# Kernel tuning notes

Measured on AMD Instinct MI355X. Metric: run time of the kernel, lower is better.

## Reference

```python
import jax, jax.numpy as jnp
import numpy as np

B, S, D = 2, 2048, 2048
NH, NKV, HD = 16, 4, 128
EPS = 1e-6


def rmsnorm(x, w, eps=EPS):
    # torch.nn.RMSNorm: x * rsqrt(mean(x^2) + eps) * weight
    ms = jnp.mean(jnp.square(x), axis=-1, keepdims=True)
    return x * jax.lax.rsqrt(ms + eps) * w


def apply_rotary_emb(x, freqs_cis):
    # x: (B, S, H, HD); freqs_cis: (S, HD//2, 2) -> pairwise complex rotation (gpt-fast style)
    xs = x.reshape(*x.shape[:-1], -1, 2)          # (B,S,H,HD//2,2)
    fc = freqs_cis[None, :, None, :, :]           # (1,S,1,HD//2,2)
    xr, xi = xs[..., 0], xs[..., 1]
    fr, fi = fc[..., 0], fc[..., 1]
    out = jnp.stack([xr * fr - xi * fi, xi * fr + xr * fi], axis=-1)
    return out.reshape(x.shape)


def setup_inputs() -> dict:
    key = jax.random.key(0)
    ks = jax.random.split(key, 4)
    x = jax.random.normal(ks[0], (B, S, D), dtype=jnp.float32)
    freqs_cis = jax.random.normal(ks[1], (S, HD // 2, 2), dtype=jnp.float32)
    wqkv = jax.random.normal(ks[2], ((NH + 2 * NKV) * HD, D), dtype=jnp.float32) * (D ** -0.5)
    wo = jax.random.normal(ks[3], (NH * HD, D), dtype=jnp.float32).T * ((NH * HD) ** -0.5)
    wo = jnp.asarray(wo)  # (D, NH*HD) torch layout (out,in)
    q_norm_w = jnp.ones((HD,), dtype=jnp.float32)
    k_norm_w = jnp.ones((HD,), dtype=jnp.float32)
    return {"x": x, "freqs_cis": freqs_cis, "wqkv": wqkv, "wo": wo,
            "q_norm_w": q_norm_w, "k_norm_w": k_norm_w}


def reference(x, freqs_cis, wqkv, wo, q_norm_w, k_norm_w):
    b, s, _ = x.shape
    q_size, kv_size = NH * HD, NKV * HD
    qkv = jnp.einsum('bsd,ed->bse', x, wqkv)  # fused QKV projection
    q, k, v = jnp.split(qkv, [q_size, q_size + kv_size], axis=-1)
    q = q.reshape(b, s, NH, HD)
    k = k.reshape(b, s, NKV, HD)
    v = v.reshape(b, s, NKV, HD)
    q = rmsnorm(q, q_norm_w)
    k = rmsnorm(k, k_norm_w)
    q = apply_rotary_emb(q, freqs_cis)
    k = apply_rotary_emb(k, freqs_cis)
    # GQA: repeat_interleave KV heads to NH
    rep = NH // NKV
    k = jnp.repeat(k, rep, axis=2)  # (b,s,NH,HD)
    v = jnp.repeat(v, rep, axis=2)
    scale = 1.0 / np.sqrt(HD)
    scores = jnp.einsum('bqhd,bkhd->bhqk', q, k) * scale
    causal = jnp.tril(jnp.ones((s, s), dtype=bool))
    scores = jnp.where(causal[None, None], scores, -jnp.inf)
    attn = jax.nn.softmax(scores, axis=-1)
    y = jnp.einsum('bhqk,bkhd->bqhd', attn, v)
    y = y.reshape(b, s, q_size)
    return jnp.einsum('bse,de->bsd', y, wo)
```

## Files before the change

### kernel.cpp

```cpp
#include <hip/hip_runtime.h>
#include <math.h>

constexpr int B_ = 2, S_ = 2048, D_ = 2048, NH_ = 16, NKV_ = 4, HD_ = 128;
constexpr int EQKV_ = (NH_ + 2 * NKV_) * HD_;
constexpr int M_ = B_ * S_;
constexpr float EPS_ = 1e-6f;
constexpr float QSCALE_ = 0.08838834764831845f;

typedef __attribute__((ext_vector_type(8))) short bf16x8;
typedef __attribute__((ext_vector_type(4))) float f32x4;
typedef __attribute__((address_space(1))) unsigned int gu32;
typedef __attribute__((address_space(3))) unsigned int lu32;

__device__ inline ushort f2bf(float f) {
    unsigned u = __float_as_uint(f);
    return (ushort)((u + 0x7FFF + ((u >> 16) & 1)) >> 16);
}

constexpr int NP_X = M_ * D_ / 4;
constexpr int NP_W = EQKV_ * D_ / 4;
constexpr int NP_O = D_ * NH_ * HD_ / 4;
__global__ __launch_bounds__(256) void pack_all(
    const float* __restrict__ x, const float* __restrict__ wqkv,
    const float* __restrict__ wo,
    ushort* __restrict__ xbf, ushort* __restrict__ wqkvbf,
    ushort* __restrict__ wobf)
{
    int i = blockIdx.x * 256 + threadIdx.x;
    const float4* src; ushort4* dst; int j;
    if (i < NP_X)                 { src = (const float4*)x;    dst = (ushort4*)xbf;    j = i; }
    else if (i < NP_X + NP_W)     { src = (const float4*)wqkv; dst = (ushort4*)wqkvbf; j = i - NP_X; }
    else if (i < NP_X + NP_W + NP_O) { src = (const float4*)wo; dst = (ushort4*)wobf;  j = i - NP_X - NP_W; }
    else return;
    float4 f = src[j];
    ushort4 u;
    u.x = f2bf(f.x); u.y = f2bf(f.y); u.z = f2bf(f.z); u.w = f2bf(f.w);
    dst[j] = u;
}

__global__ __launch_bounds__(256) void gemm_nt_bf16(
    const ushort* __restrict__ A, const ushort* __restrict__ W,
    float* __restrict__ C, int M, int N, int K)
{
    __shared__ ushort As[128 * 32];
    __shared__ ushort Bs[128 * 32];
    const int t = threadIdx.x;
    const int wave = t >> 6, lane = t & 63;
    const int nwg = gridDim.x * gridDim.y;
    int wg = blockIdx.y * gridDim.x + blockIdx.x;
    wg = (wg & 7) * (nwg >> 3) + (wg >> 3);
    const int m0 = (wg / gridDim.x) * 128, n0 = (wg % gridDim.x) * 128;
    const int wm = (wave >> 1) * 64, wn = (wave & 1) * 64;
    const int lrow = lane & 15, lquad = lane >> 4;

    f32x4 acc[4][4];
#pragma unroll
    for (int i = 0; i < 4; ++i)
#pragma unroll
        for (int j = 0; j < 4; ++j) acc[i][j] = (f32x4){0.f, 0.f, 0.f, 0.f};

    for (int k0 = 0; k0 < K; k0 += 32) {
        __syncthreads();
#pragma unroll
        for (int i = 0; i < 2; ++i) {
            int chunk = t + 256 * i;
            int row = chunk >> 2, seg = chunk & 3;
            int ubase = (wave * 64 + 256 * i) * 8;
            __builtin_amdgcn_global_load_lds(
                (const gu32*)(A + (size_t)(m0 + row) * K + k0 + seg * 8),
                (lu32*)(As + ubase), 16, 0, 0);
            __builtin_amdgcn_global_load_lds(
                (const gu32*)(W + (size_t)(n0 + row) * K + k0 + seg * 8),
                (lu32*)(Bs + ubase), 16, 0, 0);
        }
        __syncthreads();

        bf16x8 af[4], bf[4];
#pragma unroll
        for (int i = 0; i < 4; ++i) {
            af[i] = *(const bf16x8*)(As + (wm + i * 16 + lrow) * 32 + lquad * 8);
            bf[i] = *(const bf16x8*)(Bs + (wn + i * 16 + lrow) * 32 + lquad * 8);
        }
#pragma unroll
        for (int i = 0; i < 4; ++i)
#pragma unroll
            for (int j = 0; j < 4; ++j)
                acc[i][j] = __builtin_amdgcn_mfma_f32_16x16x32_bf16(
                    af[i], bf[j], acc[i][j], 0, 0, 0);
    }
#pragma unroll
    for (int i = 0; i < 4; ++i)
#pragma unroll
        for (int j = 0; j < 4; ++j) {
            float* cp = C + (size_t)(m0 + wm + i * 16 + lquad * 4) * N
                          + n0 + wn + j * 16 + lrow;
#pragma unroll
            for (int r = 0; r < 4; ++r) cp[(size_t)r * N] = acc[i][j][r];
        }
}

__global__ __launch_bounds__(256) void gemm_qkv_fused(
    const ushort* __restrict__ A,
    const ushort* __restrict__ W,
    const float* __restrict__ freqs,
    const float* __restrict__ qw, const float* __restrict__ kw,
    ushort* __restrict__ qo, ushort* __restrict__ ko, ushort* __restrict__ vo,
    int K)
{
    __shared__ __align__(16) ushort smem[128 * 136];
    __shared__ float rsbuf[256];
    ushort* As = smem;
    ushort* Bs = smem + 4096;
    ushort* Lt = smem;

    const int t = threadIdx.x;
    const int wave = t >> 6, lane = t & 63;
    const int nwg = gridDim.x * gridDim.y;
    int wg = blockIdx.y * gridDim.x + blockIdx.x;
    wg = (wg & 7) * (nwg >> 3) + (wg >> 3);
    const int m0 = (wg / gridDim.x) * 128, n0 = (wg % gridDim.x) * 128;
    const int wm = (wave >> 1) * 64, wn = (wave & 1) * 64;
    const int half = wave & 1;
    const int lrow = lane & 15, lquad = lane >> 4;
    const int head = n0 >> 7;
    const int b = m0 >> 11, s0 = m0 & (S_ - 1);

    f32x4 acc[4][4];
#pragma unroll
    for (int i = 0; i < 4; ++i)
#pragma unroll
        for (int j = 0; j < 4; ++j) acc[i][j] = (f32x4){0.f, 0.f, 0.f, 0.f};

    for (int k0 = 0; k0 < K; k0 += 32) {
        __syncthreads();
#pragma unroll
        for (int i = 0; i < 2; ++i) {
            int chunk = t + 256 * i;
            int row = chunk >> 2, seg = chunk & 3;
            int ubase = (wave * 64 + 256 * i) * 8;
            __builtin_amdgcn_global_load_lds(
                (const gu32*)(A + (size_t)(m0 + row) * K + k0 + seg * 8),
                (lu32*)(As + ubase), 16, 0, 0);
            __builtin_amdgcn_global_load_lds(
                (const gu32*)(W + (size_t)(n0 + row) * K + k0 + seg * 8),
                (lu32*)(Bs + ubase), 16, 0, 0);
        }
        __syncthreads();

        bf16x8 af[4], bf[4];
#pragma unroll
        for (int i = 0; i < 4; ++i) {
            af[i] = *(const bf16x8*)(As + (wm + i * 16 + lrow) * 32 + lquad * 8);
            bf[i] = *(const bf16x8*)(Bs + (wn + i * 16 + lrow) * 32 + lquad * 8);
        }
#pragma unroll
        for (int i = 0; i < 4; ++i)
#pragma unroll
            for (int j = 0; j < 4; ++j)
                acc[i][j] = __builtin_amdgcn_mfma_f32_16x16x32_bf16(
                    af[i], bf[j], acc[i][j], 0, 0, 0);
    }
    __syncthreads();

    float part[4][4];
    if (head < NH_ + NKV_) {
#pragma unroll
        for (int i = 0; i < 4; ++i)
#pragma unroll
            for (int r = 0; r < 4; ++r) {
                float p = acc[i][0][r] * acc[i][0][r]
                        + acc[i][1][r] * acc[i][1][r]
                        + acc[i][2][r] * acc[i][2][r]
                        + acc[i][3][r] * acc[i][3][r];
#pragma unroll
                for (int off = 1; off < 16; off <<= 1) p += __shfl_xor(p, off);
                part[i][r] = p;
                if (lrow == 0)
                    rsbuf[half * 128 + wm + i * 16 + lquad * 4 + r] = p;
            }
    }
    __syncthreads();

    if (head < NH_ + NKV_) {
        const float* nw = (head < NH_) ? qw : kw;
        float wv[4];
#pragma unroll
        for (int j = 0; j < 4; ++j) wv[j] = nw[wn + j * 16 + lrow];
#pragma unroll
        for (int i = 0; i < 4; ++i)
#pragma unroll
            for (int r = 0; r < 4; ++r) {
                const int rowid = wm + i * 16 + lquad * 4 + r;
                const int s = s0 + rowid;
                const float total = part[i][r] + rsbuf[(half ^ 1) * 128 + rowid];
                const float rs = rsqrtf(total * (1.0f / HD_) + EPS_);
#pragma unroll
                for (int j = 0; j < 4; ++j) {
                    const int d = wn + j * 16 + lrow;
                    const float xn = acc[i][j][r] * rs * wv[j];
                    const float other = __shfl_xor(xn, 1);
                    const float fr = freqs[s * HD_ + (d & ~1)];
                    const float fi = freqs[s * HD_ + (d & ~1) + 1];
                    float out = (d & 1) ? fmaf(xn, fr, other * fi)
                                        : fmaf(xn, fr, -other * fi);
                    if (head < NH_) out *= QSCALE_;
                    Lt[rowid * 136 + d] = f2bf(out);
                }
            }
    } else {
#pragma unroll
        for (int i = 0; i < 4; ++i)
#pragma unroll
            for (int j = 0; j < 4; ++j)
#pragma unroll
                for (int r = 0; r < 4; ++r)
                    Lt[(wn + j * 16 + lrow) * 136 + wm + i * 16 + lquad * 4 + r]
                        = f2bf(acc[i][j][r]);
    }
    __syncthreads();

    const int g = t >> 4, lx16 = t & 15;
    if (head < NH_) {
        ushort* dst0 = qo + ((size_t)(b * NH_ + head) * S_ + s0) * HD_;
#pragma unroll
        for (int it = 0; it < 8; ++it) {
            const int rowid = it * 16 + g;
            uint4 v = *(const uint4*)(Lt + rowid * 136 + lx16 * 8);
            *(uint4*)(dst0 + (size_t)rowid * HD_ + lx16 * 8) = v;
        }
    } else if (head < NH_ + NKV_) {
        const int kh = head - NH_;
        ushort* dst0 = ko + ((size_t)(b * NKV_ + kh) * S_ + s0) * HD_;
#pragma unroll
        for (int it = 0; it < 8; ++it) {
            const int rowid = it * 16 + g;
            uint4 v = *(const uint4*)(Lt + rowid * 136 + lx16 * 8);
            *(uint4*)(dst0 + (size_t)rowid * HD_ + lx16 * 8) = v;
        }
    } else {
        const int vh = head - (NH_ + NKV_);
        ushort* dst0 = vo + ((size_t)(b * NKV_ + vh) * HD_) * S_ + s0;
#pragma unroll
        for (int it = 0; it < 8; ++it) {
            const int rowid = it * 16 + g;
            uint4 v = *(const uint4*)(Lt + rowid * 136 + lx16 * 8);
            *(uint4*)(dst0 + (size_t)rowid * S_ + lx16 * 8) = v;
        }
    }
}

__global__ __launch_bounds__(512, 4) void flash_attn_mfma(
    const ushort* __restrict__ Q,
    const ushort* __restrict__ K,
    const ushort* __restrict__ V,
    ushort* __restrict__ Y,
    float* __restrict__ OP,
    float* __restrict__ ML)
{
    __shared__ __align__(16) ushort Ks[4 * 64 * 32];
    __shared__ __align__(16) ushort Vs[2 * 128 * 32];
    __shared__ __align__(16) ushort Ps[8 * 16 * 72];

    const int t = threadIdx.x, w = t >> 6, lane = t & 63;
    const int lx = lane & 15, quad = lane >> 4;
    const int h = blockIdx.y, b = blockIdx.z;

    const int gx = blockIdx.x;
    int qb, halfsel, tk0, tk1;
    bool split;
    if (gx < 22) {
        split = true;
        qb = 15 - (gx >> 1);
        halfsel = gx & 1;
        const int h0 = qb + 1;
        tk0 = halfsel ? h0 : 0;
        tk1 = halfsel ? 2 * qb + 2 : h0;
    } else {
        split = false;
        qb = 26 - gx;
        halfsel = 0;
        tk0 = 0;
        tk1 = 2 * qb + 2;
    }
    const int q0 = qb * 128;
    const int kvh = h >> 2;

    const int srow8 = lane >> 3, sseg8 = lane & 7;
    const int fsw = (srow8 >> 1) & 3;
    const int slotw = ((sseg8 & 3) ^ fsw) * 8;
    const int krow = w * 8 + srow8;
    const int d0 = w * 8 + srow8;
    ushort* kdst = Ks + (sseg8 >> 2) * 2048 + krow * 32 + slotw;
    ushort* vdst = Vs + (sseg8 >> 2) * 4096 + d0 * 32 + slotw;
    const ushort* ksrc = K + ((size_t)(b * NKV_ + kvh) * S_ + krow) * HD_
                           + sseg8 * 8;
    const ushort* vsrc = V + ((size_t)(b * NKV_ + kvh) * HD_ + d0) * S_
                           + sseg8 * 8;
    const int rslot = (quad ^ ((lx >> 1) & 3)) * 8;

    const ushort* qb_ = Q + ((size_t)(b * NH_ + h) * S_ + q0) * HD_;
    bf16x8 aq[4];
#pragma unroll
    for (int ks = 0; ks < 4; ++ks)
        aq[ks] = *(const bf16x8*)(qb_ + (size_t)(w * 16 + lx) * HD_ + ks * 32 + quad * 8);

    f32x4 o[8];
#pragma unroll
    for (int j = 0; j < 8; ++j) o[j] = (f32x4){0.f, 0.f, 0.f, 0.f};
    float mrow[4] = {-INFINITY, -INFINITY, -INFINITY, -INFINITY};
    float lp[4] = {0.f, 0.f, 0.f, 0.f};

    uint4 kr0, kr1, vr0, vr1;
    {
        const size_t kf = (size_t)tk0 * 64;
        kr0 = *(const uint4*)(ksrc + kf * HD_);
        kr1 = *(const uint4*)(ksrc + kf * HD_ + 64);
        vr0 = *(const uint4*)(vsrc + kf);
        vr1 = *(const uint4*)(vsrc + (size_t)64 * S_ + kf);
    }

    for (int tk = tk0; tk < tk1; ++tk) {
        const int k0 = tk * 64;
        asm volatile("s_barrier" ::: "memory");
        *(uint4*)(kdst +    0) = kr0;
        *(uint4*)(kdst + 4096) = kr1;
        *(uint4*)(vdst +    0) = vr0;
        *(uint4*)(vdst + 2048) = vr1;
        asm volatile("s_waitcnt lgkmcnt(0)" ::: "memory");
        asm volatile("s_barrier" ::: "memory");

        if (tk + 1 < tk1) {
            const size_t kf = (size_t)(k0 + 64);
            kr0 = *(const uint4*)(ksrc + kf * HD_);
            kr1 = *(const uint4*)(ksrc + kf * HD_ + 64);
            vr0 = *(const uint4*)(vsrc + kf);
            vr1 = *(const uint4*)(vsrc + (size_t)64 * S_ + kf);
        }

        f32x4 s[4];
#pragma unroll
        for (int j = 0; j < 4; ++j) s[j] = (f32x4){0.f, 0.f, 0.f, 0.f};
        __builtin_amdgcn_s_setprio(1);
#pragma unroll
        for (int ks = 0; ks < 4; ++ks) {
#pragma unroll
            for (int j = 0; j < 4; ++j) {
                bf16x8 bk = *(const bf16x8*)(Ks + ks * 2048 + (j * 16 + lx) * 32 + rslot);
                s[j] = __builtin_amdgcn_mfma_f32_16x16x32_bf16(aq[ks], bk, s[j], 0, 0, 0);
            }
        }
        __builtin_amdgcn_s_setprio(0);

        const int qrow_base = q0 + w * 16 + quad * 4;
        if (k0 + 63 > q0 + w * 16) {
#pragma unroll
            for (int reg = 0; reg < 4; ++reg) {
                const int qrow = qrow_base + reg;
#pragma unroll
                for (int j = 0; j < 4; ++j)
                    if (k0 + lx + 16 * j > qrow) s[j][reg] = -INFINITY;
            }
        }

        float rmx[4];
        bool need = false;
#pragma unroll
        for (int reg = 0; reg < 4; ++reg) {
            rmx[reg] = fmaxf(fmaxf(s[0][reg], s[1][reg]),
                             fmaxf(s[2][reg], s[3][reg]));
            need |= (rmx[reg] > mrow[reg] + 8.0f);
        }
        if (__any(need)) {
#pragma unroll
            for (int reg = 0; reg < 4; ++reg) {
                float rm = rmx[reg];
#pragma unroll
                for (int off = 1; off < 16; off <<= 1)
                    rm = fmaxf(rm, __shfl_xor(rm, off));
                const float mn = fmaxf(mrow[reg], rm);
                const float alpha = __expf(mrow[reg] - mn);
                mrow[reg] = mn;
                lp[reg] *= alpha;
#pragma unroll
                for (int j = 0; j < 8; ++j) o[j][reg] *= alpha;
            }
        }
#pragma unroll
        for (int reg = 0; reg < 4; ++reg) {
#pragma unroll
            for (int j = 0; j < 4; ++j) {
                const float p = __expf(s[j][reg] - mrow[reg]);
                lp[reg] += p;
                Ps[w * 1152 + (quad * 4 + reg) * 72 + lx + 16 * j] = f2bf(p);
            }
        }

        bf16x8 ap[2];
#pragma unroll
        for (int ks2 = 0; ks2 < 2; ++ks2)
            ap[ks2] = *(const bf16x8*)(Ps + w * 1152 + lx * 72 + ks2 * 32 + quad * 8);
        __builtin_amdgcn_s_setprio(1);
#pragma unroll
        for (int jd = 0; jd < 8; ++jd) {
#pragma unroll
            for (int ks2 = 0; ks2 < 2; ++ks2) {
                bf16x8 bv = *(const bf16x8*)(Vs + ks2 * 4096 + (jd * 16 + lx) * 32 + rslot);
                o[jd] = __builtin_amdgcn_mfma_f32_16x16x32_bf16(ap[ks2], bv, o[jd], 0, 0, 0);
            }
        }
        __builtin_amdgcn_s_setprio(0);
    }

#pragma unroll
    for (int reg = 0; reg < 4; ++reg) {
        float l = lp[reg];
#pragma unroll
        for (int off = 1; off < 16; off <<= 1) l += __shfl_xor(l, off);
        lp[reg] = l;
    }
    if (!split) {
#pragma unroll
        for (int reg = 0; reg < 4; ++reg) {
            const float inv = 1.0f / lp[reg];
            const size_t yb = (size_t)(b * S_ + q0 + w * 16 + quad * 4 + reg) * (NH_ * HD_)
                            + h * HD_ + lx;
#pragma unroll
            for (int jd = 0; jd < 8; ++jd)
                Y[yb + jd * 16] = f2bf(o[jd][reg] * inv);
        }
    } else {
        const int sp = ((b * NH_ + h) * 11 + (qb - 5)) * 2 + halfsel;
        float* mlb = ML + (size_t)sp * 256;
#pragma unroll
        for (int reg = 0; reg < 4; ++reg) {
            const int row = w * 16 + quad * 4 + reg;
            if (lx == 0) {
                mlb[row] = mrow[reg];
                mlb[128 + row] = lp[reg];
            }
            float* ob = OP + ((size_t)sp * 128 + row) * 128 + lx;
#pragma unroll
            for (int jd = 0; jd < 8; ++jd)
                ob[jd * 16] = o[jd][reg];
        }
    }
}

__global__ __launch_bounds__(256) void attn_combine(
    const float* __restrict__ OP, const float* __restrict__ ML,
    ushort* __restrict__ Y)
{
    const int gx = blockIdx.x, h = blockIdx.y, b = blockIdx.z;
    const int qb = 5 + gx;
    const int q0 = qb * 128;
    const int sp0 = ((b * NH_ + h) * 11 + gx) * 2;
    const float* ml0 = ML + (size_t)sp0 * 256;
    const float* ml1 = ML + (size_t)(sp0 + 1) * 256;
    const float* o0 = OP + (size_t)sp0 * 128 * 128;
    const float* o1 = OP + (size_t)(sp0 + 1) * 128 * 128;
    const int d = threadIdx.x & 127, rg = threadIdx.x >> 7;
#pragma unroll
    for (int r = rg; r < 128; r += 2) {
        const float m0 = ml0[r], l0 = ml0[128 + r];
        const float m1 = ml1[r], l1 = ml1[128 + r];
        const float m = fmaxf(m0, m1);
        const float w0 = __expf(m0 - m), w1 = __expf(m1 - m);
        const float inv = 1.0f / (l0 * w0 + l1 * w1);
        const float v = (o0[r * 128 + d] * w0 + o1[r * 128 + d] * w1) * inv;
        Y[((size_t)(b * S_ + q0 + r)) * (NH_ * HD_) + h * HD_ + d] = f2bf(v);
    }
}

extern "C" void kernel_launch(void* const* d_in, const int* in_sizes, int n_in,
                              void* d_out, int out_size, void* d_ws, size_t ws_size,
                              hipStream_t stream)
{
    const float* x     = (const float*)d_in[0];
    const float* freqs = (const float*)d_in[1];
    const float* wqkv  = (const float*)d_in[2];
    const float* wo    = (const float*)d_in[3];
    const float* qw    = (const float*)d_in[4];
    const float* kw    = (const float*)d_in[5];
    float* out = (float*)d_out;

    char* ws = (char*)d_ws;
    ushort* qbf    = (ushort*)(ws + 0);
    ushort* kbf    = (ushort*)(ws + 16777216);
    ushort* vtb    = (ushort*)(ws + 20971520);
    ushort* ybf    = (ushort*)(ws + 25165824);
    ushort* wobf   = (ushort*)(ws + 41943040);
    ushort* wqkvbf = (ushort*)(ws + 50331648);
    ushort* xbf    = (ushort*)(ws + 83886080);
    float*  OP     = (float*)(ws + 50331648);
    float*  ML     = (float*)(ws + 96468992);

    pack_all<<<(NP_X + NP_W + NP_O + 255) / 256, 256, 0, stream>>>(
        x, wqkv, wo, xbf, wqkvbf, wobf);
    gemm_qkv_fused<<<dim3(EQKV_ / 128, M_ / 128), 256, 0, stream>>>(
        xbf, wqkvbf, freqs, qw, kw, qbf, kbf, vtb, D_);
    flash_attn_mfma<<<dim3(27, NH_, B_), 512, 0, stream>>>(qbf, kbf, vtb, ybf,
                                                           OP, ML);
    attn_combine<<<dim3(11, NH_, B_), 256, 0, stream>>>(OP, ML, ybf);
    gemm_nt_bf16<<<dim3(D_ / 128, M_ / 128), 256, 0, stream>>>(
        ybf, wobf, out, M_, D_, NH_ * HD_);
}
```

Before: 347.5 us.

## Double GEMM K-tile to 64 with XOR-swizzled LDS layout

```diff
diff --git a/kernel.cpp b/kernel.cpp
--- a/kernel.cpp
+++ b/kernel.cpp
@@ -42,8 +42,8 @@
     const ushort* __restrict__ A, const ushort* __restrict__ W,
     float* __restrict__ C, int M, int N, int K)
 {
-    __shared__ ushort As[128 * 32];
-    __shared__ ushort Bs[128 * 32];
+    __shared__ __align__(16) ushort As[128 * 64];
+    __shared__ __align__(16) ushort Bs[128 * 64];
     const int t = threadIdx.x;
     const int wave = t >> 6, lane = t & 63;
     const int nwg = gridDim.x * gridDim.y;
@@ -53,40 +53,49 @@
     const int wm = (wave >> 1) * 64, wn = (wave & 1) * 64;
     const int lrow = lane & 15, lquad = lane >> 4;
 
+    const int srow = t >> 3;
+    const int sgo = ((t & 7) ^ (srow & 7)) * 8;
+    const ushort* Aa = A + (size_t)(m0 + srow) * K + sgo;
+    const ushort* Wa = W + (size_t)(n0 + srow) * K + sgo;
+    const int rs0 = (lquad ^ (lrow & 7)) * 8;
+    const int rs1 = rs0 ^ 32;
+
     f32x4 acc[4][4];
 #pragma unroll
     for (int i = 0; i < 4; ++i)
 #pragma unroll
         for (int j = 0; j < 4; ++j) acc[i][j] = (f32x4){0.f, 0.f, 0.f, 0.f};
 
-    for (int k0 = 0; k0 < K; k0 += 32) {
+    for (int k0 = 0; k0 < K; k0 += 64) {
         __syncthreads();
 #pragma unroll
-        for (int i = 0; i < 2; ++i) {
-            int chunk = t + 256 * i;
-            int row = chunk >> 2, seg = chunk & 3;
-            int ubase = (wave * 64 + 256 * i) * 8;
+        for (int i = 0; i < 4; ++i) {
+            const int ub = (wave * 64 + 256 * i) * 8;
             __builtin_amdgcn_global_load_lds(
-                (const gu32*)(A + (size_t)(m0 + row) * K + k0 + seg * 8),
-                (lu32*)(As + ubase), 16, 0, 0);
+                (const gu32*)(Aa + (size_t)(32 * i) * K + k0),
+                (lu32*)(As + ub), 16, 0, 0);
             __builtin_amdgcn_global_load_lds(
-                (const gu32*)(W + (size_t)(n0 + row) * K + k0 + seg * 8),
-                (lu32*)(Bs + ubase), 16, 0, 0);
+                (const gu32*)(Wa + (size_t)(32 * i) * K + k0),
+                (lu32*)(Bs + ub), 16, 0, 0);
         }
         __syncthreads();
 
-        bf16x8 af[4], bf[4];
-#pragma unroll
-        for (int i = 0; i < 4; ++i) {
-            af[i] = *(const bf16x8*)(As + (wm + i * 16 + lrow) * 32 + lquad * 8);
-            bf[i] = *(const bf16x8*)(Bs + (wn + i * 16 + lrow) * 32 + lquad * 8);
-        }
-#pragma unroll
-        for (int i = 0; i < 4; ++i)
-#pragma unroll
-            for (int j = 0; j < 4; ++j)
-                acc[i][j] = __builtin_amdgcn_mfma_f32_16x16x32_bf16(
-                    af[i], bf[j], acc[i][j], 0, 0, 0);
+#pragma unroll
+        for (int ks = 0; ks < 2; ++ks) {
+            const int so = ks ? rs1 : rs0;
+            bf16x8 af[4], bf[4];
+#pragma unroll
+            for (int i = 0; i < 4; ++i) {
+                af[i] = *(const bf16x8*)(As + (wm + i * 16 + lrow) * 64 + so);
+                bf[i] = *(const bf16x8*)(Bs + (wn + i * 16 + lrow) * 64 + so);
+            }
+#pragma unroll
+            for (int i = 0; i < 4; ++i)
+#pragma unroll
+                for (int j = 0; j < 4; ++j)
+                    acc[i][j] = __builtin_amdgcn_mfma_f32_16x16x32_bf16(
+                        af[i], bf[j], acc[i][j], 0, 0, 0);
+        }
     }
 #pragma unroll
     for (int i = 0; i < 4; ++i)
@@ -107,10 +116,10 @@
     ushort* __restrict__ qo, ushort* __restrict__ ko, ushort* __restrict__ vo,
     int K)
 {
-    __shared__ __align__(16) ushort smem[128 * 136];
+    __shared__ __align__(16) ushort smem[17408];
     __shared__ float rsbuf[256];
     ushort* As = smem;
-    ushort* Bs = smem + 4096;
+    ushort* Bs = smem + 8192;
     ushort* Lt = smem;
 
     const int t = threadIdx.x;
@@ -125,40 +134,49 @@
     const int head = n0 >> 7;
     const int b = m0 >> 11, s0 = m0 & (S_ - 1);
 
+    const int srow = t >> 3;
+    const int sgo = ((t & 7) ^ (srow & 7)) * 8;
+    const ushort* Aa = A + (size_t)(m0 + srow) * K + sgo;
+    const ushort* Wa = W + (size_t)(n0 + srow) * K + sgo;
+    const int rs0 = (lquad ^ (lrow & 7)) * 8;
+    const int rs1 = rs0 ^ 32;
+
     f32x4 acc[4][4];
 #pragma unroll
     for (int i = 0; i < 4; ++i)
 #pragma unroll
         for (int j = 0; j < 4; ++j) acc[i][j] = (f32x4){0.f, 0.f, 0.f, 0.f};
 
-    for (int k0 = 0; k0 < K; k0 += 32) {
+    for (int k0 = 0; k0 < K; k0 += 64) {
         __syncthreads();
 #pragma unroll
-        for (int i = 0; i < 2; ++i) {
-            int chunk = t + 256 * i;
-            int row = chunk >> 2, seg = chunk & 3;
-            int ubase = (wave * 64 + 256 * i) * 8;
+        for (int i = 0; i < 4; ++i) {
+            const int ub = (wave * 64 + 256 * i) * 8;
             __builtin_amdgcn_global_load_lds(
-                (const gu32*)(A + (size_t)(m0 + row) * K + k0 + seg * 8),
-                (lu32*)(As + ubase), 16, 0, 0);
+                (const gu32*)(Aa + (size_t)(32 * i) * K + k0),
+                (lu32*)(As + ub), 16, 0, 0);
             __builtin_amdgcn_global_load_lds(
-                (const gu32*)(W + (size_t)(n0 + row) * K + k0 + seg * 8),
-                (lu32*)(Bs + ubase), 16, 0, 0);
+                (const gu32*)(Wa + (size_t)(32 * i) * K + k0),
+                (lu32*)(Bs + ub), 16, 0, 0);
         }
         __syncthreads();
 
-        bf16x8 af[4], bf[4];
-#pragma unroll
-        for (int i = 0; i < 4; ++i) {
-            af[i] = *(const bf16x8*)(As + (wm + i * 16 + lrow) * 32 + lquad * 8);
-            bf[i] = *(const bf16x8*)(Bs + (wn + i * 16 + lrow) * 32 + lquad * 8);
-        }
-#pragma unroll
-        for (int i = 0; i < 4; ++i)
-#pragma unroll
-            for (int j = 0; j < 4; ++j)
-                acc[i][j] = __builtin_amdgcn_mfma_f32_16x16x32_bf16(
-                    af[i], bf[j], acc[i][j], 0, 0, 0);
+#pragma unroll
+        for (int ks = 0; ks < 2; ++ks) {
+            const int so = ks ? rs1 : rs0;
+            bf16x8 af[4], bf[4];
+#pragma unroll
+            for (int i = 0; i < 4; ++i) {
+                af[i] = *(const bf16x8*)(As + (wm + i * 16 + lrow) * 64 + so);
+                bf[i] = *(const bf16x8*)(Bs + (wn + i * 16 + lrow) * 64 + so);
+            }
+#pragma unroll
+            for (int i = 0; i < 4; ++i)
+#pragma unroll
+                for (int j = 0; j < 4; ++j)
+                    acc[i][j] = __builtin_amdgcn_mfma_f32_16x16x32_bf16(
+                        af[i], bf[j], acc[i][j], 0, 0, 0);
+        }
     }
     __syncthreads();
 
```

Result: no change. 343.2 us (-1.2%).
